# Kernel optimization log

Hardware: AMD Instinct MI355X
Metric: run time of the kernel (lower is better)

## Reference

```python
import jax, jax.numpy as jnp
import numpy as np

D = 256          # in_dim == out_dim for both layers
B, S = 8, 1024   # batch, seq_len
EPS = 1e-5       # LayerNorm eps (torch default)


def _layernorm(x, g, b):
    mu = jnp.mean(x, axis=-1, keepdims=True)
    var = jnp.var(x, axis=-1, keepdims=True)
    return (x - mu) * jax.lax.rsqrt(var + EPS) * g + b


def _periods(d):
    i = jnp.arange(d, dtype=jnp.float32)
    # periods[i, j] = i*d + j + 2
    return i[:, None] * d + i[None, :] + 2.0


def _layer(x, M, P, g, b, positions):
    # x: [B, S, in_dim] -> [B, S, out_dim]
    x_trans = jnp.einsum('bsj,ij->bsi', x, M)      # x @ M.T
    x_trans = _layernorm(x_trans, g, b)
    k = positions.astype(jnp.float32)[:, None, None]            # [S,1,1]
    phi = jnp.cos(2.0 * jnp.pi * k / _periods(D)[None])         # [S,D,D]
    Mk = P[None] * phi                                          # [S,D,D]
    Nk = jnp.einsum('bsj,sij->bsi', x_trans, Mk)
    # use_residual='separate' with in_dim==out_dim -> Identity residual
    return Nk + x


def setup_inputs() -> dict:
    key = jax.random.key(0)
    ks = jax.random.split(key, 5)
    seq = jax.random.normal(ks[0], (B, S, D), dtype=jnp.float32)
    M1 = jax.random.uniform(ks[1], (D, D), jnp.float32, -0.5, 0.5)
    P1 = jax.random.uniform(ks[2], (D, D), jnp.float32, -0.1, 0.1)
    M2 = jax.random.uniform(ks[3], (D, D), jnp.float32, -0.5, 0.5)
    P2 = jax.random.uniform(ks[4], (D, D), jnp.float32, -0.1, 0.1)
    g1 = jnp.ones((D,), jnp.float32); b1 = jnp.zeros((D,), jnp.float32)
    g2 = jnp.ones((D,), jnp.float32); b2 = jnp.zeros((D,), jnp.float32)
    return {"seq": seq, "M1": M1, "P1": P1, "g1": g1, "b1": b1,
            "M2": M2, "P2": P2, "g2": g2, "b2": b2}


def reference(seq, M1, P1, g1, b1, M2, P2, g2, b2):
    positions = jnp.arange(S)
    x = _layer(seq, M1, P1, g1, b1, positions)
    x = _layer(x, M2, P2, g2, b2, positions)
    return x
```

## Files before the change

kernel.cpp:

```cpp
#include <hip/hip_runtime.h>

#define DD 256
#define BB 8
#define SS 1024
#define XSTRIDE 264

typedef _Float16 half8  __attribute__((ext_vector_type(8)));
typedef _Float16 half2t __attribute__((ext_vector_type(2)));
typedef __fp16   fp16x2 __attribute__((ext_vector_type(2)));
typedef __attribute__((ext_vector_type(4))) float float4v;

__device__ __forceinline__ half2t pkrtz(float a, float b) {
    union { fp16x2 f; half2t h; } cv;
    cv.f = __builtin_amdgcn_cvt_pkrtz(a, b);
    return cv.h;
}

__global__ void cast_mats_f16(const float* __restrict__ M1, const float* __restrict__ P1,
                              const float* __restrict__ M2, const float* __restrict__ P2,
                              unsigned* __restrict__ ws)
{
    int id  = blockIdx.x * 256 + threadIdx.x;
    int mat = id >> 15;
    int off = id & 32767;
    const float2* src = (mat == 0) ? (const float2*)M1
                      : (mat == 1) ? (const float2*)P1
                      : (mat == 2) ? (const float2*)M2 : (const float2*)P2;
    float2 v = src[off];
    union { half2t h; unsigned u; } cv;
    cv.h = pkrtz(v.x, v.y);
    ws[id] = cv.u;
}

template<bool PRECAST>
__global__ __launch_bounds__(512, 4)
void fused_hierddpm(const float* __restrict__ seq,
                    const float* __restrict__ M1, const float* __restrict__ P1,
                    const float* __restrict__ g1, const float* __restrict__ be1,
                    const float* __restrict__ M2, const float* __restrict__ P2,
                    const float* __restrict__ g2, const float* __restrict__ be2,
                    const _Float16* __restrict__ wsh,
                    float* __restrict__ out)
{
    __shared__ __align__(16) _Float16 xsb[16][XSTRIDE];
    __shared__ __align__(16) _Float16 xtb[16][XSTRIDE];
    __shared__ float stats[8][16][2];

    const int tid  = threadIdx.x;
    const int w    = tid >> 6;
    const int lane = tid & 63;
    const int l15  = lane & 15;
    const int quad = lane >> 4;
    const int s0   = blockIdx.x * 2;
    const float k0 = (float)s0, k1 = (float)(s0 + 1);

    {
        const float4* seq4 = (const float4*)seq;
        #pragma unroll
        for (int u = 0; u < 2; ++u) {
            int v  = tid + 512 * u;
            int sl = v >> 9;
            int rm = v & 511;
            int b  = rm >> 6, j4 = rm & 63;
            float4 x = seq4[((size_t)b * SS + s0 + sl) * 64 + j4];
            half2t* dst = (half2t*)&xsb[sl * 8 + b][4 * j4];
            dst[0] = pkrtz(x.x, x.y);
            dst[1] = pkrtz(x.z, x.w);
        }
    }

    float res[2][4];
    {
        const int sl = quad >> 1;
        #pragma unroll
        for (int t = 0; t < 2; ++t) {
            int col = 16 * (2 * w + t) + l15;
            #pragma unroll
            for (int reg = 0; reg < 4; ++reg) {
                int b = (quad * 4 + reg) & 7;
                res[t][reg] = seq[((size_t)b * SS + s0 + sl) * DD + col];
            }
        }
    }
    __syncthreads();

    #pragma unroll 1
    for (int layer = 0; layer < 2; ++layer) {
        const float* M  = layer ? M2  : M1;
        const float* P  = layer ? P2  : P1;
        const float* g  = layer ? g2  : g1;
        const float* be = layer ? be2 : be1;
        const _Float16* Mh = wsh + (size_t)layer * 131072;
        const _Float16* Ph = Mh + 65536;

        float4v acc1[2];
        acc1[0] = (float4v){0.f, 0.f, 0.f, 0.f};
        acc1[1] = (float4v){0.f, 0.f, 0.f, 0.f};

        #pragma unroll 1
        for (int kt = 0; kt < 8; ++kt) {
            half8 a = *(const half8*)&xsb[l15][kt * 32 + quad * 8];
            #pragma unroll
            for (int t = 0; t < 2; ++t) {
                int n = 16 * (2 * w + t) + l15;
                half8 bfrag;
                if (PRECAST) {
                    bfrag = *(const half8*)(Mh + (size_t)n * DD + kt * 32 + quad * 8);
                } else {
                    const float4* Mr = (const float4*)M +
                        ((size_t)n * 64 + kt * 8 + quad * 2);
                    float4 m0 = Mr[0], m1 = Mr[1];
                    union { half8 h; half2t h2[4]; } bb;
                    bb.h2[0] = pkrtz(m0.x, m0.y);
                    bb.h2[1] = pkrtz(m0.z, m0.w);
                    bb.h2[2] = pkrtz(m1.x, m1.y);
                    bb.h2[3] = pkrtz(m1.z, m1.w);
                    bfrag = bb.h;
                }
                acc1[t] = __builtin_amdgcn_mfma_f32_16x16x32_f16(a, bfrag, acc1[t], 0, 0, 0);
            }
        }

        {
            #pragma unroll
            for (int reg = 0; reg < 4; ++reg) {
                float sm = acc1[0][reg] + acc1[1][reg];
                float sq = fmaf(acc1[0][reg], acc1[0][reg], acc1[1][reg] * acc1[1][reg]);
                #pragma unroll
                for (int off = 1; off < 16; off <<= 1) {
                    sm += __shfl_xor(sm, off, 64);
                    sq += __shfl_xor(sq, off, 64);
                }
                if (l15 == 0) {
                    stats[w][quad * 4 + reg][0] = sm;
                    stats[w][quad * 4 + reg][1] = sq;
                }
            }
        }
        __syncthreads();
        {
            float mu[4], rs[4];
            #pragma unroll
            for (int reg = 0; reg < 4; ++reg) {
                int m = quad * 4 + reg;
                float sm = 0.f, sq = 0.f;
                #pragma unroll
                for (int ww = 0; ww < 8; ++ww) {
                    sm += stats[ww][m][0];
                    sq += stats[ww][m][1];
                }
                float mm = sm * (1.f / DD);
                mu[reg] = mm;
                rs[reg] = rsqrtf(sq * (1.f / DD) - mm * mm + 1e-5f);
            }
            #pragma unroll
            for (int t = 0; t < 2; ++t) {
                int col = 16 * (2 * w + t) + l15;
                float gv = g[col], bv = be[col];
                #pragma unroll
                for (int reg = 0; reg < 4; ++reg) {
                    float v = fmaf((acc1[t][reg] - mu[reg]) * rs[reg], gv, bv);
                    xtb[quad * 4 + reg][col] = (_Float16)v;
                }
            }
        }
        __syncthreads();

        float4v accS[2][2];
        #pragma unroll
        for (int sl = 0; sl < 2; ++sl)
            #pragma unroll
            for (int t = 0; t < 2; ++t) accS[sl][t] = (float4v){0.f, 0.f, 0.f, 0.f};

        #pragma unroll 1
        for (int kt = 0; kt < 8; ++kt) {
            half8 a = *(const half8*)&xtb[l15][kt * 32 + quad * 8];
            #pragma unroll
            for (int t = 0; t < 2; ++t) {
                const int n = 16 * (2 * w + t) + l15;
                union { half8 h; half2t h2[4]; } pv;
                if (PRECAST) {
                    pv.h = *(const half8*)(Ph + (size_t)n * DD + kt * 32 + quad * 8);
                } else {
                    const float4* Pr = (const float4*)P +
                        ((size_t)n * 64 + kt * 8 + quad * 2);
                    float4 p0 = Pr[0], p1 = Pr[1];
                    pv.h2[0] = pkrtz(p0.x, p0.y);
                    pv.h2[1] = pkrtz(p0.z, p0.w);
                    pv.h2[2] = pkrtz(p1.x, p1.y);
                    pv.h2[3] = pkrtz(p1.z, p1.w);
                }
                const float pbase = (float)(n * DD + kt * 32 + quad * 8 + 2);
                union { half8 h; half2t h2[4]; } b0, b1;
                #pragma unroll
                for (int e = 0; e < 4; ++e) {
                    float ia = __builtin_amdgcn_rcpf(pbase + (float)(2 * e));
                    float ib = __builtin_amdgcn_rcpf(pbase + (float)(2 * e + 1));
                    half2t c0 = pkrtz(
                        __builtin_amdgcn_cosf(__builtin_amdgcn_fractf(k0 * ia)),
                        __builtin_amdgcn_cosf(__builtin_amdgcn_fractf(k0 * ib)));
                    half2t c1 = pkrtz(
                        __builtin_amdgcn_cosf(__builtin_amdgcn_fractf(k1 * ia)),
                        __builtin_amdgcn_cosf(__builtin_amdgcn_fractf(k1 * ib)));
                    b0.h2[e] = pv.h2[e] * c0;
                    b1.h2[e] = pv.h2[e] * c1;
                }
                accS[0][t] = __builtin_amdgcn_mfma_f32_16x16x32_f16(a, b0.h, accS[0][t], 0, 0, 0);
                accS[1][t] = __builtin_amdgcn_mfma_f32_16x16x32_f16(a, b1.h, accS[1][t], 0, 0, 0);
            }
        }

        #pragma unroll
        for (int t = 0; t < 2; ++t) {
            int col = 16 * (2 * w + t) + l15;
            float4v av = (quad < 2) ? accS[0][t] : accS[1][t];
            int sl = quad >> 1;
            #pragma unroll
            for (int reg = 0; reg < 4; ++reg) {
                int m = quad * 4 + reg;
                int b = m & 7;
                float val = av[reg] + res[t][reg];
                if (layer == 0) {
                    res[t][reg] = val;
                    xsb[m][col] = (_Float16)val;
                } else {
                    out[((size_t)b * SS + s0 + sl) * DD + col] = val;
                }
            }
        }
        if (layer == 0) __syncthreads();
    }
}

extern "C" void kernel_launch(void* const* d_in, const int* in_sizes, int n_in,
                              void* d_out, int out_size, void* d_ws, size_t ws_size,
                              hipStream_t stream)
{
    const float* seq = (const float*)d_in[0];
    const float* M1  = (const float*)d_in[1];
    const float* P1  = (const float*)d_in[2];
    const float* g1  = (const float*)d_in[3];
    const float* b1  = (const float*)d_in[4];
    const float* M2  = (const float*)d_in[5];
    const float* P2  = (const float*)d_in[6];
    const float* g2  = (const float*)d_in[7];
    const float* b2  = (const float*)d_in[8];
    float* out = (float*)d_out;

    if (ws_size >= 512 * 1024) {
        cast_mats_f16<<<512, 256, 0, stream>>>(M1, P1, M2, P2, (unsigned*)d_ws);
        fused_hierddpm<true><<<SS / 2, 512, 0, stream>>>(
            seq, M1, P1, g1, b1, M2, P2, g2, b2, (const _Float16*)d_ws, out);
    } else {
        fused_hierddpm<false><<<SS / 2, 512, 0, stream>>>(
            seq, M1, P1, g1, b1, M2, P2, g2, b2, nullptr, out);
    }
}
```

Baseline: 122.2 us.

## Precompute fragment-ordered weight tables and reciprocal-period table in a prep kernel

The prep kernel now writes M and P in half precision, already laid out in MFMA fragment order so each lane's load is contiguous. It also writes a per-element table of reciprocal periods, so the main kernel no longer runs rcp for every weight element in every block. The second GEMM loop is unrolled by two. In exchange the main kernel reads an extra 256 KB table per layer, which adds memory traffic and more workspace (1 MB total).

```diff
diff --git a/kernel.cpp b/kernel.cpp
--- a/kernel.cpp
+++ b/kernel.cpp
@@ -5,6 +5,11 @@
 #define SS 1024
 #define XSTRIDE 264
 
+#define LAYER_BYTES 524288
+#define PTAB_OFF    131072
+#define ITAB_OFF    262144
+#define WS_NEEDED   (2 * LAYER_BYTES)
+
 typedef _Float16 half8  __attribute__((ext_vector_type(8)));
 typedef _Float16 half2t __attribute__((ext_vector_type(2)));
 typedef __fp16   fp16x2 __attribute__((ext_vector_type(2)));
@@ -16,30 +21,53 @@
     return cv.h;
 }
 
-__global__ void cast_mats_f16(const float* __restrict__ M1, const float* __restrict__ P1,
-                              const float* __restrict__ M2, const float* __restrict__ P2,
-                              unsigned* __restrict__ ws)
+__global__ void build_tabs(const float* __restrict__ M1, const float* __restrict__ P1,
+                           const float* __restrict__ M2, const float* __restrict__ P2,
+                           char* __restrict__ ws)
 {
-    int id  = blockIdx.x * 256 + threadIdx.x;
-    int mat = id >> 15;
-    int off = id & 32767;
-    const float2* src = (mat == 0) ? (const float2*)M1
-                      : (mat == 1) ? (const float2*)P1
-                      : (mat == 2) ? (const float2*)M2 : (const float2*)P2;
-    float2 v = src[off];
-    union { half2t h; unsigned u; } cv;
-    cv.h = pkrtz(v.x, v.y);
-    ws[id] = cv.u;
-}
-
-template<bool PRECAST>
+    int gid   = blockIdx.x * 256 + threadIdx.x;
+    int layer = gid >> 13;
+    int gi    = gid & 8191;
+    int idx   = gi >> 6;
+    int lane  = gi & 63;
+    int kt    = idx >> 4;
+    int wt    = idx & 15;
+    int l15   = lane & 15, quad = lane >> 4;
+    int n     = 16 * wt + l15;
+    int j0    = kt * 32 + quad * 8;
+
+    const float* Msrc = layer ? M2 : M1;
+    const float* Psrc = layer ? P2 : P1;
+
+    union { half8 h; half2t h2[4]; } mh, ph;
+    float iv[8];
+    #pragma unroll
+    for (int e = 0; e < 4; ++e) {
+        float ma = Msrc[(size_t)n * DD + j0 + 2 * e];
+        float mb = Msrc[(size_t)n * DD + j0 + 2 * e + 1];
+        float pa = Psrc[(size_t)n * DD + j0 + 2 * e];
+        float pb = Psrc[(size_t)n * DD + j0 + 2 * e + 1];
+        mh.h2[e] = pkrtz(ma, mb);
+        ph.h2[e] = pkrtz(pa, pb);
+        iv[2 * e]     = 1.0f / (float)(n * DD + j0 + 2 * e + 2);
+        iv[2 * e + 1] = 1.0f / (float)(n * DD + j0 + 2 * e + 3);
+    }
+    char* base = ws + (size_t)layer * LAYER_BYTES;
+    ((half8*)base)[gi]                       = mh.h;
+    ((half8*)(base + PTAB_OFF))[gi]          = ph.h;
+    float4* it = (float4*)(base + ITAB_OFF);
+    it[2 * gi]     = make_float4(iv[0], iv[1], iv[2], iv[3]);
+    it[2 * gi + 1] = make_float4(iv[4], iv[5], iv[6], iv[7]);
+}
+
+template<bool TABS>
 __global__ __launch_bounds__(512, 4)
 void fused_hierddpm(const float* __restrict__ seq,
                     const float* __restrict__ M1, const float* __restrict__ P1,
                     const float* __restrict__ g1, const float* __restrict__ be1,
                     const float* __restrict__ M2, const float* __restrict__ P2,
                     const float* __restrict__ g2, const float* __restrict__ be2,
-                    const _Float16* __restrict__ wsh,
+                    const char* __restrict__ ws,
                     float* __restrict__ out)
 {
     __shared__ __align__(16) _Float16 xsb[16][XSTRIDE];
@@ -90,8 +118,10 @@
         const float* P  = layer ? P2  : P1;
         const float* g  = layer ? g2  : g1;
         const float* be = layer ? be2 : be1;
-        const _Float16* Mh = wsh + (size_t)layer * 131072;
-        const _Float16* Ph = Mh + 65536;
+        const char*  lbase = ws + (size_t)layer * LAYER_BYTES;
+        const half8*  Mtab = (const half8*)lbase;
+        const half8*  Ptab = (const half8*)(lbase + PTAB_OFF);
+        const float4* Itab = (const float4*)(lbase + ITAB_OFF);
 
         float4v acc1[2];
         acc1[0] = (float4v){0.f, 0.f, 0.f, 0.f};
@@ -102,11 +132,11 @@
             half8 a = *(const half8*)&xsb[l15][kt * 32 + quad * 8];
             #pragma unroll
             for (int t = 0; t < 2; ++t) {
-                int n = 16 * (2 * w + t) + l15;
                 half8 bfrag;
-                if (PRECAST) {
-                    bfrag = *(const half8*)(Mh + (size_t)n * DD + kt * 32 + quad * 8);
+                if (TABS) {
+                    bfrag = Mtab[(kt * 16 + 2 * w + t) * 64 + lane];
                 } else {
+                    int n = 16 * (2 * w + t) + l15;
                     const float4* Mr = (const float4*)M +
                         ((size_t)n * 64 + kt * 8 + quad * 2);
                     float4 m0 = Mr[0], m1 = Mr[1];
@@ -172,16 +202,21 @@
             #pragma unroll
             for (int t = 0; t < 2; ++t) accS[sl][t] = (float4v){0.f, 0.f, 0.f, 0.f};
 
-        #pragma unroll 1
+        #pragma unroll 2
         for (int kt = 0; kt < 8; ++kt) {
             half8 a = *(const half8*)&xtb[l15][kt * 32 + quad * 8];
             #pragma unroll
             for (int t = 0; t < 2; ++t) {
-                const int n = 16 * (2 * w + t) + l15;
                 union { half8 h; half2t h2[4]; } pv;
-                if (PRECAST) {
-                    pv.h = *(const half8*)(Ph + (size_t)n * DD + kt * 32 + quad * 8);
+                float iv[8];
+                if (TABS) {
+                    int gi = (kt * 16 + 2 * w + t) * 64 + lane;
+                    pv.h = Ptab[gi];
+                    float4 i0 = Itab[2 * gi], i1 = Itab[2 * gi + 1];
+                    iv[0] = i0.x; iv[1] = i0.y; iv[2] = i0.z; iv[3] = i0.w;
+                    iv[4] = i1.x; iv[5] = i1.y; iv[6] = i1.z; iv[7] = i1.w;
                 } else {
+                    int n = 16 * (2 * w + t) + l15;
                     const float4* Pr = (const float4*)P +
                         ((size_t)n * 64 + kt * 8 + quad * 2);
                     float4 p0 = Pr[0], p1 = Pr[1];
@@ -189,13 +224,15 @@
                     pv.h2[1] = pkrtz(p0.z, p0.w);
                     pv.h2[2] = pkrtz(p1.x, p1.y);
                     pv.h2[3] = pkrtz(p1.z, p1.w);
-                }
-                const float pbase = (float)(n * DD + kt * 32 + quad * 8 + 2);
+                    float pbase = (float)(n * DD + kt * 32 + quad * 8 + 2);
+                    #pragma unroll
+                    for (int e = 0; e < 8; ++e)
+                        iv[e] = __builtin_amdgcn_rcpf(pbase + (float)e);
+                }
                 union { half8 h; half2t h2[4]; } b0, b1;
                 #pragma unroll
                 for (int e = 0; e < 4; ++e) {
-                    float ia = __builtin_amdgcn_rcpf(pbase + (float)(2 * e));
-                    float ib = __builtin_amdgcn_rcpf(pbase + (float)(2 * e + 1));
+                    float ia = iv[2 * e], ib = iv[2 * e + 1];
                     half2t c0 = pkrtz(
                         __builtin_amdgcn_cosf(__builtin_amdgcn_fractf(k0 * ia)),
                         __builtin_amdgcn_cosf(__builtin_amdgcn_fractf(k0 * ib)));
@@ -247,10 +284,10 @@
     const float* b2  = (const float*)d_in[8];
     float* out = (float*)d_out;
 
-    if (ws_size >= 512 * 1024) {
-        cast_mats_f16<<<512, 256, 0, stream>>>(M1, P1, M2, P2, (unsigned*)d_ws);
+    if (ws_size >= WS_NEEDED) {
+        build_tabs<<<64, 256, 0, stream>>>(M1, P1, M2, P2, (char*)d_ws);
         fused_hierddpm<true><<<SS / 2, 512, 0, stream>>>(
-            seq, M1, P1, g1, b1, M2, P2, g2, b2, (const _Float16*)d_ws, out);
+            seq, M1, P1, g1, b1, M2, P2, g2, b2, (const char*)d_ws, out);
     } else {
         fused_hierddpm<false><<<SS / 2, 512, 0, stream>>>(
             seq, M1, P1, g1, b1, M2, P2, g2, b2, nullptr, out);
```

Result: faster. 114.4 us (-6.4%).
